# Kernel optimization log

Hardware: AMD Instinct MI355X
Metric: run time of the kernel (lower is better)

The kernel has to match this reference:

```python
import jax, jax.numpy as jnp
import numpy as np

K_MAX = 64      # config.k_max
N_HASH = 8      # LSH hash bits per table


def setup_inputs() -> dict:
    key = jax.random.key(0)
    kq, kk, kw = jax.random.split(key, 3)
    B, L, D = 4, 2048, 64
    query = jax.random.normal(kq, (B, L, D), dtype=jnp.float32)
    key_t = jax.random.normal(kk, (B, L, D), dtype=jnp.float32)
    W = jax.random.normal(kw, (D, N_HASH), dtype=jnp.float32)  # LSH projection
    return {"query": query, "key": key_t, "W": W, "head_idx": 0}


def _hash_code(x, W):
    # binary_quantize then LSH hash: sign bits of random projection, packed to one int code
    x_bin = jnp.where(x > 0, 1.0, 0.0)                      # [B,L,D]
    bits = (jnp.einsum('bld,dh->blh', x_bin, W) > 0)        # [B,L,H] bool
    weights = (2 ** jnp.arange(N_HASH, dtype=jnp.int32))    # pack bits -> bucket id
    return jnp.sum(bits.astype(jnp.int32) * weights, axis=-1)  # [B,L] int32


def reference(query, key, W, head_idx):
    B, L, _ = query.shape
    q_code = _hash_code(query, W)   # [B,L]
    k_code = _hash_code(key, W)     # [B,L]
    # hash-equality match matrix [B, Lq, Lk] (== .all(dim=2) on hash bits)
    matches = q_code[:, :, None] == k_code[:, None, :]
    idx = jnp.arange(L, dtype=jnp.int32)
    # non-matches get sentinel L so the k_max smallest indices are the first matches
    cand_keys = jnp.where(matches, idx[None, None, :], L)   # [B,L,L]
    neg_top, _ = jax.lax.top_k(-cand_keys, K_MAX)           # k_max smallest indices
    cand = -neg_top                                          # ascending first-match order
    return jnp.where(cand == L, -1, cand).astype(jnp.int64)  # [B,L,k_max], -1 padded
```

## Files before the change

### kernel.cpp

```cpp
#include <hip/hip_runtime.h>

#define D 64
#define H 8
#define LSEQ 2048
#define KMAX 64
#define NCODES 256

__global__ void __launch_bounds__(64)
code_kernel(const float* __restrict__ query,
            const float* __restrict__ key,
            const float* __restrict__ W,
            int* __restrict__ q_code,
            unsigned char* __restrict__ kperm,
            int n_pos) {
    __shared__ float Ws[D * H];
    for (int i = threadIdx.x; i < D * H; i += blockDim.x) Ws[i] = W[i];
    __syncthreads();

    int t = blockIdx.x * blockDim.x + threadIdx.x;
    if (t >= 2 * n_pos) return;

    const float* xp = (t < n_pos) ? (query + (size_t)t * D)
                                  : (key + (size_t)(t - n_pos) * D);
    float4 s0 = {0.f, 0.f, 0.f, 0.f};
    float4 s1 = {0.f, 0.f, 0.f, 0.f};

#pragma unroll
    for (int d4 = 0; d4 < D / 4; ++d4) {
        float4 xv = ((const float4*)xp)[d4];
        const float* x4 = (const float*)&xv;
#pragma unroll
        for (int k = 0; k < 4; ++k) {
            int d = d4 * 4 + k;
            float4 w0 = *(const float4*)&Ws[d * H + 0];
            float4 w1 = *(const float4*)&Ws[d * H + 4];
            bool p = x4[k] > 0.0f;
            s0.x += p ? w0.x : 0.0f;
            s0.y += p ? w0.y : 0.0f;
            s0.z += p ? w0.z : 0.0f;
            s0.w += p ? w0.w : 0.0f;
            s1.x += p ? w1.x : 0.0f;
            s1.y += p ? w1.y : 0.0f;
            s1.z += p ? w1.z : 0.0f;
            s1.w += p ? w1.w : 0.0f;
        }
    }
    int c = 0;
    c |= (s0.x > 0.0f) ? 1   : 0;
    c |= (s0.y > 0.0f) ? 2   : 0;
    c |= (s0.z > 0.0f) ? 4   : 0;
    c |= (s0.w > 0.0f) ? 8   : 0;
    c |= (s1.x > 0.0f) ? 16  : 0;
    c |= (s1.y > 0.0f) ? 32  : 0;
    c |= (s1.z > 0.0f) ? 64  : 0;
    c |= (s1.w > 0.0f) ? 128 : 0;

    if (t < n_pos) {
        q_code[t] = c;
    } else {
        int kk = t - n_pos;
        int b    = kk >> 11;
        int l    = kk & (LSEQ - 1);
        int lane = l & 63;
        int j    = (l >> 6) & 3;
        int i4   = l >> 8;
        kperm[(b << 11) + (i4 << 8) + (lane << 2) + j] = (unsigned char)c;
    }
}

__global__ void __launch_bounds__(256)
scan_emit_kernel(const int* __restrict__ q_code,
                 const unsigned int* __restrict__ kperm,
                 int* __restrict__ out) {
    __shared__ int rows[4][KMAX];
    int wave = threadIdx.x >> 6;
    int lane = threadIdx.x & 63;
    int q = blockIdx.x * 4 + wave;
    int b = q >> 11;

    int c = q_code[q];
    const unsigned int* kp = kperm + (size_t)b * (LSEQ / 4) + lane;
    int* row = rows[wave];
    row[lane] = -1;

    unsigned int v[LSEQ / 256];
#pragma unroll
    for (int i = 0; i < LSEQ / 256; ++i) v[i] = kp[i * 64];

    unsigned long long lt_mask = (lane == 63) ? 0x7FFFFFFFFFFFFFFFull
                                              : ((1ull << lane) - 1ull);
    int base = 0;
#pragma unroll
    for (int i = 0; i < LSEQ / 256; ++i) {
        unsigned int w = v[i];
#pragma unroll
        for (int j = 0; j < 4; ++j) {
            int ci = (int)((w >> (8 * j)) & 0xFFu);
            unsigned long long mask = __ballot(ci == c);
            if (ci == c) {
                int rank = base + __popcll(mask & lt_mask);
                if (rank < KMAX) row[rank] = i * 256 + j * 64 + lane;
            }
            base += __popcll(mask);
        }
    }
    out[(size_t)q * KMAX + lane] = row[lane];
}

extern "C" void kernel_launch(void* const* d_in, const int* in_sizes, int n_in,
                              void* d_out, int out_size, void* d_ws, size_t ws_size,
                              hipStream_t stream) {
    const float* query = (const float*)d_in[0];
    const float* key   = (const float*)d_in[1];
    const float* W     = (const float*)d_in[2];

    int n_pos = in_sizes[0] / D;
    (void)ws_size;

    int* q_code = (int*)d_ws;
    unsigned char* kperm = (unsigned char*)(q_code + n_pos);

    {
        int total = 2 * n_pos;
        code_kernel<<<(total + 63) / 64, 64, 0, stream>>>(query, key, W,
                                                          q_code, kperm, n_pos);
    }
    {
        scan_emit_kernel<<<n_pos / 4, 256, 0, stream>>>(q_code,
                                                        (const unsigned int*)kperm,
                                                        (int*)d_out);
    }
}
```

Before: 72.81 us.

## Replace per-key ballot scan with per-lane bitmask and wave prefix sum

Keys are stored in natural order and each lane takes a contiguous chunk of 32 key codes, loaded as two uint4s. The lane builds a 32-bit match mask locally, then a shuffle-based prefix scan across the wave gives each lane its output offset before it writes the match indices in order. This replaces 32 ballot-and-popcount steps per query with local compares plus a 6-step shuffle scan. The trade-off is a data-dependent while loop per lane, which can diverge when match counts are uneven.

```diff
diff --git a/kernel.cpp b/kernel.cpp
--- a/kernel.cpp
+++ b/kernel.cpp
@@ -11,7 +11,7 @@
             const float* __restrict__ key,
             const float* __restrict__ W,
             int* __restrict__ q_code,
-            unsigned char* __restrict__ kperm,
+            unsigned char* __restrict__ kcode,
             int n_pos) {
     __shared__ float Ws[D * H];
     for (int i = threadIdx.x; i < D * H; i += blockDim.x) Ws[i] = W[i];
@@ -58,19 +58,13 @@
     if (t < n_pos) {
         q_code[t] = c;
     } else {
-        int kk = t - n_pos;
-        int b    = kk >> 11;
-        int l    = kk & (LSEQ - 1);
-        int lane = l & 63;
-        int j    = (l >> 6) & 3;
-        int i4   = l >> 8;
-        kperm[(b << 11) + (i4 << 8) + (lane << 2) + j] = (unsigned char)c;
+        kcode[t - n_pos] = (unsigned char)c;
     }
 }
 
 __global__ void __launch_bounds__(256)
 scan_emit_kernel(const int* __restrict__ q_code,
-                 const unsigned int* __restrict__ kperm,
+                 const unsigned char* __restrict__ kcode,
                  int* __restrict__ out) {
     __shared__ int rows[4][KMAX];
     int wave = threadIdx.x >> 6;
@@ -78,32 +72,53 @@
     int q = blockIdx.x * 4 + wave;
     int b = q >> 11;
 
-    int c = q_code[q];
-    const unsigned int* kp = kperm + (size_t)b * (LSEQ / 4) + lane;
+    unsigned int cu = (unsigned int)q_code[q];
+    const uint4* kp4 = (const uint4*)(kcode + (size_t)b * LSEQ) + lane * 2;
     int* row = rows[wave];
     row[lane] = -1;
 
-    unsigned int v[LSEQ / 256];
+    uint4 v0 = kp4[0];
+    uint4 v1 = kp4[1];
+
+    unsigned int m = 0;
+    {
+        const unsigned int* w0 = (const unsigned int*)&v0;
+        const unsigned int* w1 = (const unsigned int*)&v1;
 #pragma unroll
-    for (int i = 0; i < LSEQ / 256; ++i) v[i] = kp[i * 64];
-
-    unsigned long long lt_mask = (lane == 63) ? 0x7FFFFFFFFFFFFFFFull
-                                              : ((1ull << lane) - 1ull);
-    int base = 0;
+        for (int u = 0; u < 4; ++u) {
+            unsigned int w = w0[u];
 #pragma unroll
-    for (int i = 0; i < LSEQ / 256; ++i) {
-        unsigned int w = v[i];
+            for (int j = 0; j < 4; ++j)
+                if (((w >> (8 * j)) & 0xFFu) == cu) m |= 1u << (u * 4 + j);
+        }
 #pragma unroll
-        for (int j = 0; j < 4; ++j) {
-            int ci = (int)((w >> (8 * j)) & 0xFFu);
-            unsigned long long mask = __ballot(ci == c);
-            if (ci == c) {
-                int rank = base + __popcll(mask & lt_mask);
-                if (rank < KMAX) row[rank] = i * 256 + j * 64 + lane;
-            }
-            base += __popcll(mask);
+        for (int u = 0; u < 4; ++u) {
+            unsigned int w = w1[u];
+#pragma unroll
+            for (int j = 0; j < 4; ++j)
+                if (((w >> (8 * j)) & 0xFFu) == cu) m |= 1u << (16 + u * 4 + j);
         }
     }
+    int cnt = __popc(m);
+
+    int inc = cnt;
+#pragma unroll
+    for (int d = 1; d < 64; d <<= 1) {
+        int n = __shfl_up(inc, d);
+        if (lane >= d) inc += n;
+    }
+    int base = inc - cnt;
+
+    unsigned int mm = m;
+    int k = 0;
+    while (mm) {
+        int tz = __builtin_ctz(mm);
+        mm &= mm - 1;
+        int r = base + k;
+        if (r < KMAX) row[r] = lane * 32 + tz;
+        ++k;
+    }
+
     out[(size_t)q * KMAX + lane] = row[lane];
 }
 
@@ -118,16 +133,15 @@
     (void)ws_size;
 
     int* q_code = (int*)d_ws;
-    unsigned char* kperm = (unsigned char*)(q_code + n_pos);
+    unsigned char* kcode = (unsigned char*)(q_code + n_pos);
 
     {
         int total = 2 * n_pos;
         code_kernel<<<(total + 63) / 64, 64, 0, stream>>>(query, key, W,
-                                                          q_code, kperm, n_pos);
+                                                          q_code, kcode, n_pos);
     }
     {
-        scan_emit_kernel<<<n_pos / 4, 256, 0, stream>>>(q_code,
-                                                        (const unsigned int*)kperm,
+        scan_emit_kernel<<<n_pos / 4, 256, 0, stream>>>(q_code, kcode,
                                                         (int*)d_out);
     }
 }
```

Measured after the change: 71.01 us. -2.5%, faster.
